# Optimization experiments

Measured on AMD Instinct MI355X. Metric: run time of the kernel, lower is better.

The kernel has to match this reference:

```python
import jax, jax.numpy as jnp
import numpy as np

B, S, H, I = 2, 2048, 2048, 8192

def setup_inputs() -> dict:
    key = jax.random.key(0)
    k1, k2, k3, k4 = jax.random.split(key, 4)
    x = jax.random.normal(k1, (B, S, H), dtype=jnp.float32)
    gate_w = jax.random.normal(k2, (I, H), dtype=jnp.float32) * 0.02
    up_w = jax.random.normal(k3, (I, H), dtype=jnp.float32) * 0.02
    down_w = jax.random.normal(k4, (H, I), dtype=jnp.float32) * 0.02
    return {"x": x, "gate_w": gate_w, "up_w": up_w, "down_w": down_w}

def reference(x, gate_w, up_w, down_w):
    # SwiGLU FFN forward. In the torch module the hybrid compression only
    # affects activations SAVED for backward; forward output is exact F.linear.
    h_gate = jnp.einsum('bsh,ih->bsi', x, gate_w)   # (B,S,I)
    h_up = jnp.einsum('bsh,ih->bsi', x, up_w)       # (B,S,I)
    h_mid = jax.nn.silu(h_gate) * h_up              # (B,S,I)
    y = jnp.einsum('bsi,hi->bsh', h_mid, down_w)    # (B,S,H)
    return y
```

## Files before the change

### kernel.cpp

```cpp
#include <hip/hip_runtime.h>
#include <hip/hip_bf16.h>
#include <stdint.h>

typedef __attribute__((ext_vector_type(4))) float f32x4;
typedef __attribute__((ext_vector_type(8))) short short8;

__device__ __forceinline__ unsigned short f32_to_bf16_rne(float f) {
  union { float f; unsigned int u; } v; v.f = f;
  unsigned int u = v.u;
  unsigned int r = u + 0x7fffu + ((u >> 16) & 1u);
  return (unsigned short)(r >> 16);
}

#define GLOAD16(gp, lp)                                                 \
  __builtin_amdgcn_global_load_lds(                                     \
      (const __attribute__((address_space(1))) void*)(const void*)(gp), \
      (__attribute__((address_space(3))) void*)(void*)(lp), 16, 0, 0)

#define BAR() __builtin_amdgcn_s_barrier()
#define WAIT_LGKM0() asm volatile("s_waitcnt lgkmcnt(0)" ::: "memory")
#define WAIT_VM8() asm volatile("s_waitcnt vmcnt(8)" ::: "memory")
#define WAIT_VM0() asm volatile("s_waitcnt vmcnt(0)" ::: "memory")


__global__ __launch_bounds__(256) void cvt_f32_bf16(const float* __restrict__ in,
                                                    unsigned short* __restrict__ out,
                                                    int n4) {
  int i = blockIdx.x * 256 + threadIdx.x;
  int stride = gridDim.x * 256;
  for (; i < n4; i += stride) {
    float4 v = reinterpret_cast<const float4*>(in)[i];
    ushort4 o;
    o.x = f32_to_bf16_rne(v.x);
    o.y = f32_to_bf16_rne(v.y);
    o.z = f32_to_bf16_rne(v.z);
    o.w = f32_to_bf16_rne(v.w);
    reinterpret_cast<ushort4*>(out)[i] = o;
  }
}

__global__ __launch_bounds__(256) void pack_gateup(const float* __restrict__ g,
                                                   const float* __restrict__ u,
                                                   unsigned short* __restrict__ out) {
  const int n = 16384 * 512;
  int idx = blockIdx.x * 256 + threadIdx.x;
  for (; idx < n; idx += gridDim.x * 256) {
    int R = idx >> 9, h4 = idx & 511;
    int grp = R >> 5, s = R & 31;
    const float* src = (s < 16 ? g : u) + (((size_t)(grp * 16 + (s & 15))) << 11) + (h4 << 2);
    float4 v = *reinterpret_cast<const float4*>(src);
    ushort4 o;
    o.x = f32_to_bf16_rne(v.x);
    o.y = f32_to_bf16_rne(v.y);
    o.z = f32_to_bf16_rne(v.z);
    o.w = f32_to_bf16_rne(v.w);
    *reinterpret_cast<ushort4*>(out + ((size_t)idx << 2)) = o;
  }
}

__global__ __launch_bounds__(256) void reduce_add(const float* __restrict__ a,
                                                  const float* __restrict__ b,
                                                  float* __restrict__ o, int n4) {
  int i = blockIdx.x * 256 + threadIdx.x;
  for (; i < n4; i += gridDim.x * 256) {
    float4 x = reinterpret_cast<const float4*>(a)[i];
    float4 y = reinterpret_cast<const float4*>(b)[i];
    float4 z;
    z.x = x.x + y.x; z.y = x.y + y.y; z.z = x.z + y.z; z.w = x.w + y.w;
    reinterpret_cast<float4*>(o)[i] = z;
  }
}


#define MFMA_Q(MH, NH)                                                        \
  do {                                                                        \
    _Pragma("unroll") for (int kh = 0; kh < 2; ++kh) {                        \
      _Pragma("unroll") for (int mi = 0; mi < 4; ++mi) {                      \
        _Pragma("unroll") for (int ni = 0; ni < 2; ++ni) {                    \
          acc[(MH)*4 + mi][(NH)*2 + ni] =                                     \
              __builtin_amdgcn_mfma_f32_16x16x32_bf16(                        \
                  a[mi][kh], b[(NH)*2 + ni][kh],                              \
                  acc[(MH)*4 + mi][(NH)*2 + ni], 0, 0, 0);                    \
        }                                                                     \
      }                                                                       \
    }                                                                         \
  } while (0)

#define STAGE(MAT, BUF, H, T)                                                 \
  do {                                                                        \
    const unsigned short* p0_ =                                               \
        MAT##base + (size_t)((H)*128 + r0) * ld##MAT + (size_t)(T)*64 + c0;   \
    const unsigned short* p1_ =                                               \
        MAT##base + (size_t)((H)*128 + r1) * ld##MAT + (size_t)(T)*64 + c1;   \
    GLOAD16(p0_, &s##MAT[BUF][H][off0 >> 1]);                                 \
    GLOAD16(p1_, &s##MAT[BUF][H][(off0 >> 1) + 512]);                         \
  } while (0)

#define LDA(dst, BUF, MI, KH)                                                 \
  {                                                                           \
    int lb_ = ((MI)*16 + frow) * 128 + (KH)*64 + kg * 16;                     \
    int ph_ = lb_ ^ ((frow & 7) << 4);                                        \
    dst = *reinterpret_cast<const short8*>(                                   \
        reinterpret_cast<const char*>(&sA[BUF][wr][0]) + ph_);                \
  }

#define LDB(dst, BUF, NI, KH)                                                 \
  {                                                                           \
    int lb_ = ((wc & 1) * 64 + (NI)*16 + frow) * 128 + (KH)*64 + kg * 16;     \
    int ph_ = lb_ ^ ((frow & 7) << 4);                                        \
    dst = *reinterpret_cast<const short8*>(                                   \
        reinterpret_cast<const char*>(&sB[BUF][wc >> 1][0]) + ph_);           \
  }

template <int EPI>
__global__ __launch_bounds__(512, 2) void gemm8p(
    const unsigned short* __restrict__ A, const unsigned short* __restrict__ B,
    void* __restrict__ Cout, int K, int ldA, int ldB, int Nout, size_t zstride,
    int nbm, int nbn) {
  __shared__ unsigned short sA[2][2][128 * 64];
  __shared__ unsigned short sB[2][2][128 * 64];

  const int t = threadIdx.x;
  const int wv = t >> 6, ln = t & 63;
  const int wr = wv >> 2, wc = wv & 3;
  const int frow = ln & 15, kg = ln >> 4;

  const int r = blockIdx.x;
  const int swz = (r & 7) * (gridDim.x >> 3) + (r >> 3);
  const int bm = swz % nbm;
  const int rest = swz / nbm;
  const int bn = rest % nbn;
  const int bz = rest / nbn;

  A += (size_t)bz * K;
  B += (size_t)bz * K;

  const int off0 = wv * 2048 + ln * 16;
  const int off1 = off0 + 1024;
  const int s0 = off0 ^ (((off0 >> 7) & 7) << 4);
  const int s1 = off1 ^ (((off1 >> 7) & 7) << 4);
  const int r0 = s0 >> 7, c0 = (s0 & 127) >> 1;
  const int r1 = s1 >> 7, c1 = (s1 & 127) >> 1;

  const unsigned short* Abase = A + (size_t)(bm * 256) * ldA;
  const unsigned short* Bbase = B + (size_t)(bn * 256) * ldB;

  f32x4 acc[8][4] = {};
  short8 a[4][2], b[4][2];

  const int NT = K >> 6;

  STAGE(A, 0, 0, 0); STAGE(A, 0, 1, 0);
  STAGE(B, 0, 0, 0); STAGE(B, 0, 1, 0);
  STAGE(A, 1, 0, 1); STAGE(A, 1, 1, 1);
  STAGE(B, 1, 0, 1); STAGE(B, 1, 1, 1);
  WAIT_VM8();
  BAR();

  for (int tt = 0; tt < NT; ++tt) {
    const int buf = tt & 1;
#pragma unroll
    for (int mi = 0; mi < 4; ++mi) { LDA(a[mi][0], buf, mi, 0); LDA(a[mi][1], buf, mi, 1); }
#pragma unroll
    for (int ni = 0; ni < 2; ++ni) { LDB(b[ni][0], buf, ni, 0); LDB(b[ni][1], buf, ni, 1); }
    BAR(); WAIT_LGKM0();
    __builtin_amdgcn_s_setprio(1); MFMA_Q(0, 0); __builtin_amdgcn_s_setprio(0);
    BAR();
#pragma unroll
    for (int ni = 2; ni < 4; ++ni) { LDB(b[ni][0], buf, ni, 0); LDB(b[ni][1], buf, ni, 1); }
    BAR(); WAIT_LGKM0();
    __builtin_amdgcn_s_setprio(1); MFMA_Q(0, 1); __builtin_amdgcn_s_setprio(0);
    BAR();
#pragma unroll
    for (int mi = 0; mi < 4; ++mi) { LDA(a[mi][0], buf, mi + 4, 0); LDA(a[mi][1], buf, mi + 4, 1); }
    if (tt + 2 < NT) { STAGE(B, buf, 0, tt + 2); STAGE(B, buf, 1, tt + 2); }
    BAR(); WAIT_LGKM0();
    __builtin_amdgcn_s_setprio(1); MFMA_Q(1, 0); __builtin_amdgcn_s_setprio(0);
    BAR();
    if (tt + 2 < NT) { STAGE(A, buf, 0, tt + 2); STAGE(A, buf, 1, tt + 2); }
    BAR(); WAIT_LGKM0();
    __builtin_amdgcn_s_setprio(1); MFMA_Q(1, 1); __builtin_amdgcn_s_setprio(0);
    if (tt < NT - 1) {
      if (tt + 2 < NT) { WAIT_VM8(); } else { WAIT_VM0(); }
    }
    BAR();
  }

  if (EPI == 0) {
    float* C = reinterpret_cast<float*>(Cout) + (size_t)bz * zstride;
    const int rb = bm * 256 + wr * 128 + kg * 4;
    const int cb = bn * 256 + wc * 64 + frow;
#pragma unroll
    for (int mi = 0; mi < 8; ++mi)
#pragma unroll
      for (int ni = 0; ni < 4; ++ni)
#pragma unroll
        for (int j = 0; j < 4; ++j)
          C[(size_t)(rb + mi * 16 + j) * Nout + (cb + ni * 16)] = acc[mi][ni][j];
  } else {
    unsigned short* Hm = reinterpret_cast<unsigned short*>(Cout);
    const int rb = bm * 256 + wr * 128 + kg * 4;
    const int cb = bn * 128 + wc * 32 + frow;
#pragma unroll
    for (int mi = 0; mi < 8; ++mi)
#pragma unroll
      for (int p = 0; p < 2; ++p)
#pragma unroll
        for (int j = 0; j < 4; ++j) {
          float gg = acc[mi][2 * p][j];
          float uu = acc[mi][2 * p + 1][j];
          float h = gg * uu * __builtin_amdgcn_rcpf(1.0f + __expf(-gg));
          Hm[(size_t)(rb + mi * 16 + j) * Nout + (cb + p * 16)] = f32_to_bf16_rne(h);
        }
  }
}


extern "C" void kernel_launch(void* const* d_in, const int* in_sizes, int n_in,
                              void* d_out, int out_size, void* d_ws, size_t ws_size,
                              hipStream_t stream) {
  const float* x      = (const float*)d_in[0];
  const float* gate_w = (const float*)d_in[1];
  const float* up_w   = (const float*)d_in[2];
  const float* down_w = (const float*)d_in[3];
  float* y = (float*)d_out;

  const int Mtok = 4096, H = 2048, I = 8192;

  unsigned short* x_bf = (unsigned short*)d_ws;
  unsigned short* Bcat = x_bf + (size_t)Mtok * H;
  unsigned short* d_bf = Bcat + (size_t)2 * I * H;
  unsigned short* h_bf = d_bf + (size_t)H * I;
  float* part = (float*)Bcat;

  cvt_f32_bf16<<<2048, 256, 0, stream>>>(down_w, d_bf, (H * I) / 4);
  cvt_f32_bf16<<<2048, 256, 0, stream>>>(x, x_bf, (Mtok * H) / 4);
  pack_gateup<<<2048, 256, 0, stream>>>(gate_w, up_w, Bcat);

  gemm8p<1><<<dim3(1024), 512, 0, stream>>>(
      x_bf, Bcat, h_bf, H, H, H, I, 0, Mtok / 256, (2 * I) / 256);

  gemm8p<0><<<dim3(256), 512, 0, stream>>>(
      h_bf, d_bf, part, I / 2, I, I, H, (size_t)Mtok * H, Mtok / 256, H / 256);

  reduce_add<<<2048, 256, 0, stream>>>(part, part + (size_t)Mtok * H, y,
                                       (Mtok * H) / 4);
}
```

Baseline: 457.6 us.

## Switch GEMM to 32x32x16 MFMA tiles and fuse conversion kernels into one prep

Replaces the 16x16x32 bf16 MFMA inner loop with 32x32x16 MFMAs, changing the LDS fragment loads, the accumulator layout and both epilogues. The gate/up interleave in the packed weight changes from groups of 16 rows to groups of 32 to match the wider N fragment. The three f32-to-bf16 conversion launches are merged into a single prep kernel. The intent is fewer MFMA issues and LDS reads per FLOP, plus less launch overhead. The risk is bank conflicts in the new fragment load pattern and a changed register footprint.

```diff
diff --git a/kernel.cpp b/kernel.cpp
--- a/kernel.cpp
+++ b/kernel.cpp
@@ -3,6 +3,7 @@
 #include <stdint.h>
 
 typedef __attribute__((ext_vector_type(4))) float f32x4;
+typedef __attribute__((ext_vector_type(16))) float f32x16;
 typedef __attribute__((ext_vector_type(8))) short short8;
 
 __device__ __forceinline__ unsigned short f32_to_bf16_rne(float f) {
@@ -22,39 +23,40 @@
 #define WAIT_VM8() asm volatile("s_waitcnt vmcnt(8)" ::: "memory")
 #define WAIT_VM0() asm volatile("s_waitcnt vmcnt(0)" ::: "memory")
 
-
-__global__ __launch_bounds__(256) void cvt_f32_bf16(const float* __restrict__ in,
-                                                    unsigned short* __restrict__ out,
-                                                    int n4) {
+__global__ __launch_bounds__(256) void prep(
+    const float* __restrict__ x, const float* __restrict__ g,
+    const float* __restrict__ u, const float* __restrict__ dw,
+    unsigned short* __restrict__ x_bf, unsigned short* __restrict__ d_bf,
+    unsigned short* __restrict__ Bcat) {
+  const int NX4 = 2097152;
+  const int ND4 = 4194304;
+  const int NP4 = 8388608;
+  const int total = NX4 + ND4 + NP4;
   int i = blockIdx.x * 256 + threadIdx.x;
-  int stride = gridDim.x * 256;
-  for (; i < n4; i += stride) {
-    float4 v = reinterpret_cast<const float4*>(in)[i];
-    ushort4 o;
-    o.x = f32_to_bf16_rne(v.x);
-    o.y = f32_to_bf16_rne(v.y);
-    o.z = f32_to_bf16_rne(v.z);
-    o.w = f32_to_bf16_rne(v.w);
-    reinterpret_cast<ushort4*>(out)[i] = o;
-  }
-}
-
-__global__ __launch_bounds__(256) void pack_gateup(const float* __restrict__ g,
-                                                   const float* __restrict__ u,
-                                                   unsigned short* __restrict__ out) {
-  const int n = 16384 * 512;
-  int idx = blockIdx.x * 256 + threadIdx.x;
-  for (; idx < n; idx += gridDim.x * 256) {
-    int R = idx >> 9, h4 = idx & 511;
-    int grp = R >> 5, s = R & 31;
-    const float* src = (s < 16 ? g : u) + (((size_t)(grp * 16 + (s & 15))) << 11) + (h4 << 2);
+  for (; i < total; i += gridDim.x * 256) {
+    const float* src;
+    unsigned short* dst;
+    if (i < NX4) {
+      src = x + ((size_t)i << 2);
+      dst = x_bf + ((size_t)i << 2);
+    } else if (i < NX4 + ND4) {
+      int j = i - NX4;
+      src = dw + ((size_t)j << 2);
+      dst = d_bf + ((size_t)j << 2);
+    } else {
+      int j = i - NX4 - ND4;
+      int R = j >> 9, h4 = j & 511;
+      int grp = R >> 6, s = R & 63;
+      src = (s < 32 ? g : u) + (((size_t)(grp * 32 + (s & 31))) << 11) + (h4 << 2);
+      dst = Bcat + ((size_t)j << 2);
+    }
     float4 v = *reinterpret_cast<const float4*>(src);
     ushort4 o;
     o.x = f32_to_bf16_rne(v.x);
     o.y = f32_to_bf16_rne(v.y);
     o.z = f32_to_bf16_rne(v.z);
     o.w = f32_to_bf16_rne(v.w);
-    *reinterpret_cast<ushort4*>(out + ((size_t)idx << 2)) = o;
+    *reinterpret_cast<ushort4*>(dst) = o;
   }
 }
 
@@ -72,16 +74,12 @@
 }
 
 
-#define MFMA_Q(MH, NH)                                                        \
+#define MFMA_P(MH, NH)                                                        \
   do {                                                                        \
-    _Pragma("unroll") for (int kh = 0; kh < 2; ++kh) {                        \
-      _Pragma("unroll") for (int mi = 0; mi < 4; ++mi) {                      \
-        _Pragma("unroll") for (int ni = 0; ni < 2; ++ni) {                    \
-          acc[(MH)*4 + mi][(NH)*2 + ni] =                                     \
-              __builtin_amdgcn_mfma_f32_16x16x32_bf16(                        \
-                  a[mi][kh], b[(NH)*2 + ni][kh],                              \
-                  acc[(MH)*4 + mi][(NH)*2 + ni], 0, 0, 0);                    \
-        }                                                                     \
+    _Pragma("unroll") for (int ks = 0; ks < 4; ++ks) {                        \
+      _Pragma("unroll") for (int mp = 0; mp < 2; ++mp) {                      \
+        acc[(MH)*2 + mp][NH] = __builtin_amdgcn_mfma_f32_32x32x16_bf16(       \
+            a[mp][ks], b[NH][ks], acc[(MH)*2 + mp][NH], 0, 0, 0);             \
       }                                                                       \
     }                                                                         \
   } while (0)
@@ -96,18 +94,20 @@
     GLOAD16(p1_, &s##MAT[BUF][H][(off0 >> 1) + 512]);                         \
   } while (0)
 
-#define LDA(dst, BUF, MI, KH)                                                 \
+#define LDA32(dst, BUF, MI, KS)                                               \
   {                                                                           \
-    int lb_ = ((MI)*16 + frow) * 128 + (KH)*64 + kg * 16;                     \
-    int ph_ = lb_ ^ ((frow & 7) << 4);                                        \
+    int row_ = (MI)*32 + (ln & 31);                                           \
+    int lb_ = row_ * 128 + (KS)*32 + ((ln >> 5) << 4);                        \
+    int ph_ = lb_ ^ ((row_ & 7) << 4);                                        \
     dst = *reinterpret_cast<const short8*>(                                   \
         reinterpret_cast<const char*>(&sA[BUF][wr][0]) + ph_);                \
   }
 
-#define LDB(dst, BUF, NI, KH)                                                 \
+#define LDB32(dst, BUF, NI, KS)                                               \
   {                                                                           \
-    int lb_ = ((wc & 1) * 64 + (NI)*16 + frow) * 128 + (KH)*64 + kg * 16;     \
-    int ph_ = lb_ ^ ((frow & 7) << 4);                                        \
+    int row_ = (wc & 1) * 64 + (NI)*32 + (ln & 31);                           \
+    int lb_ = row_ * 128 + (KS)*32 + ((ln >> 5) << 4);                        \
+    int ph_ = lb_ ^ ((row_ & 7) << 4);                                        \
     dst = *reinterpret_cast<const short8*>(                                   \
         reinterpret_cast<const char*>(&sB[BUF][wc >> 1][0]) + ph_);           \
   }
@@ -123,7 +123,6 @@
   const int t = threadIdx.x;
   const int wv = t >> 6, ln = t & 63;
   const int wr = wv >> 2, wc = wv & 3;
-  const int frow = ln & 15, kg = ln >> 4;
 
   const int r = blockIdx.x;
   const int swz = (r & 7) * (gridDim.x >> 3) + (r >> 3);
@@ -145,8 +144,8 @@
   const unsigned short* Abase = A + (size_t)(bm * 256) * ldA;
   const unsigned short* Bbase = B + (size_t)(bn * 256) * ldB;
 
-  f32x4 acc[8][4] = {};
-  short8 a[4][2], b[4][2];
+  f32x16 acc[4][2] = {};
+  short8 a[2][4], b[2][4];
 
   const int NT = K >> 6;
 
@@ -160,26 +159,30 @@
   for (int tt = 0; tt < NT; ++tt) {
     const int buf = tt & 1;
 #pragma unroll
-    for (int mi = 0; mi < 4; ++mi) { LDA(a[mi][0], buf, mi, 0); LDA(a[mi][1], buf, mi, 1); }
-#pragma unroll
-    for (int ni = 0; ni < 2; ++ni) { LDB(b[ni][0], buf, ni, 0); LDB(b[ni][1], buf, ni, 1); }
-    BAR(); WAIT_LGKM0();
-    __builtin_amdgcn_s_setprio(1); MFMA_Q(0, 0); __builtin_amdgcn_s_setprio(0);
-    BAR();
-#pragma unroll
-    for (int ni = 2; ni < 4; ++ni) { LDB(b[ni][0], buf, ni, 0); LDB(b[ni][1], buf, ni, 1); }
-    BAR(); WAIT_LGKM0();
-    __builtin_amdgcn_s_setprio(1); MFMA_Q(0, 1); __builtin_amdgcn_s_setprio(0);
-    BAR();
-#pragma unroll
-    for (int mi = 0; mi < 4; ++mi) { LDA(a[mi][0], buf, mi + 4, 0); LDA(a[mi][1], buf, mi + 4, 1); }
+    for (int mp = 0; mp < 2; ++mp)
+#pragma unroll
+      for (int ks = 0; ks < 4; ++ks) LDA32(a[mp][ks], buf, mp, ks);
+#pragma unroll
+    for (int ks = 0; ks < 4; ++ks) LDB32(b[0][ks], buf, 0, ks);
+    BAR(); WAIT_LGKM0();
+    __builtin_amdgcn_s_setprio(1); MFMA_P(0, 0); __builtin_amdgcn_s_setprio(0);
+    BAR();
+#pragma unroll
+    for (int ks = 0; ks < 4; ++ks) LDB32(b[1][ks], buf, 1, ks);
+    BAR(); WAIT_LGKM0();
+    __builtin_amdgcn_s_setprio(1); MFMA_P(0, 1); __builtin_amdgcn_s_setprio(0);
+    BAR();
+#pragma unroll
+    for (int mp = 0; mp < 2; ++mp)
+#pragma unroll
+      for (int ks = 0; ks < 4; ++ks) LDA32(a[mp][ks], buf, 2 + mp, ks);
     if (tt + 2 < NT) { STAGE(B, buf, 0, tt + 2); STAGE(B, buf, 1, tt + 2); }
     BAR(); WAIT_LGKM0();
-    __builtin_amdgcn_s_setprio(1); MFMA_Q(1, 0); __builtin_amdgcn_s_setprio(0);
+    __builtin_amdgcn_s_setprio(1); MFMA_P(1, 0); __builtin_amdgcn_s_setprio(0);
     BAR();
     if (tt + 2 < NT) { STAGE(A, buf, 0, tt + 2); STAGE(A, buf, 1, tt + 2); }
     BAR(); WAIT_LGKM0();
-    __builtin_amdgcn_s_setprio(1); MFMA_Q(1, 1); __builtin_amdgcn_s_setprio(0);
+    __builtin_amdgcn_s_setprio(1); MFMA_P(1, 1); __builtin_amdgcn_s_setprio(0);
     if (tt < NT - 1) {
       if (tt + 2 < NT) { WAIT_VM8(); } else { WAIT_VM0(); }
     }
@@ -188,30 +191,31 @@
 
   if (EPI == 0) {
     float* C = reinterpret_cast<float*>(Cout) + (size_t)bz * zstride;
-    const int rb = bm * 256 + wr * 128 + kg * 4;
-    const int cb = bn * 256 + wc * 64 + frow;
-#pragma unroll
-    for (int mi = 0; mi < 8; ++mi)
-#pragma unroll
-      for (int ni = 0; ni < 4; ++ni)
-#pragma unroll
-        for (int j = 0; j < 4; ++j)
-          C[(size_t)(rb + mi * 16 + j) * Nout + (cb + ni * 16)] = acc[mi][ni][j];
+    const int rb = bm * 256 + wr * 128 + 4 * (ln >> 5);
+    const int cb = bn * 256 + wc * 64 + (ln & 31);
+#pragma unroll
+    for (int mi = 0; mi < 4; ++mi)
+#pragma unroll
+      for (int nh = 0; nh < 2; ++nh)
+#pragma unroll
+        for (int reg = 0; reg < 16; ++reg) {
+          int row = rb + mi * 32 + (reg & 3) + 8 * (reg >> 2);
+          C[(size_t)row * Nout + cb + nh * 32] = acc[mi][nh][reg];
+        }
   } else {
     unsigned short* Hm = reinterpret_cast<unsigned short*>(Cout);
-    const int rb = bm * 256 + wr * 128 + kg * 4;
-    const int cb = bn * 128 + wc * 32 + frow;
-#pragma unroll
-    for (int mi = 0; mi < 8; ++mi)
-#pragma unroll
-      for (int p = 0; p < 2; ++p)
-#pragma unroll
-        for (int j = 0; j < 4; ++j) {
-          float gg = acc[mi][2 * p][j];
-          float uu = acc[mi][2 * p + 1][j];
-          float h = gg * uu * __builtin_amdgcn_rcpf(1.0f + __expf(-gg));
-          Hm[(size_t)(rb + mi * 16 + j) * Nout + (cb + p * 16)] = f32_to_bf16_rne(h);
-        }
+    const int rb = bm * 256 + wr * 128 + 4 * (ln >> 5);
+    const int cb = bn * 128 + wc * 32 + (ln & 31);
+#pragma unroll
+    for (int mi = 0; mi < 4; ++mi)
+#pragma unroll
+      for (int reg = 0; reg < 16; ++reg) {
+        float gg = acc[mi][0][reg];
+        float uu = acc[mi][1][reg];
+        float h = gg * uu * __builtin_amdgcn_rcpf(1.0f + __expf(-gg));
+        int row = rb + mi * 32 + (reg & 3) + 8 * (reg >> 2);
+        Hm[(size_t)row * Nout + cb] = f32_to_bf16_rne(h);
+      }
   }
 }
 
@@ -233,9 +237,7 @@
   unsigned short* h_bf = d_bf + (size_t)H * I;
   float* part = (float*)Bcat;
 
-  cvt_f32_bf16<<<2048, 256, 0, stream>>>(down_w, d_bf, (H * I) / 4);
-  cvt_f32_bf16<<<2048, 256, 0, stream>>>(x, x_bf, (Mtok * H) / 4);
-  pack_gateup<<<2048, 256, 0, stream>>>(gate_w, up_w, Bcat);
+  prep<<<2048, 256, 0, stream>>>(x, gate_w, up_w, down_w, x_bf, d_bf, Bcat);
 
   gemm8p<1><<<dim3(1024), 512, 0, stream>>>(
       x_bf, Bcat, h_bf, H, H, H, I, 0, Mtok / 256, (2 * I) / 256);
```

New measurement: 501.2 us. 1.1x slower.

## Make gate/up GEMM persistent across tiles and merge prep conversions into one kernel

Applied to the files above, without the earlier changes.

The three fp32-to-bf16 conversion kernels become a single prep kernel, which saves two launches. The first GEMM now runs a persistent grid of 256 workgroups. Each workgroup processes 4 consecutive output tiles in one continuous K loop, so loads for the next tile's first k-slices are issued while the current tile finishes and its epilogue runs. The trade-off is that the epilogue now sits inside the main loop, which adds register pressure and branches, and tile assignment per workgroup changes L2 locality.

```diff
diff --git a/kernel.cpp b/kernel.cpp
--- a/kernel.cpp
+++ b/kernel.cpp
@@ -22,39 +22,40 @@
 #define WAIT_VM8() asm volatile("s_waitcnt vmcnt(8)" ::: "memory")
 #define WAIT_VM0() asm volatile("s_waitcnt vmcnt(0)" ::: "memory")
 
-
-__global__ __launch_bounds__(256) void cvt_f32_bf16(const float* __restrict__ in,
-                                                    unsigned short* __restrict__ out,
-                                                    int n4) {
+__global__ __launch_bounds__(256) void prep(
+    const float* __restrict__ x, const float* __restrict__ g,
+    const float* __restrict__ u, const float* __restrict__ dw,
+    unsigned short* __restrict__ x_bf, unsigned short* __restrict__ d_bf,
+    unsigned short* __restrict__ Bcat) {
+  const int NX4 = 2097152;
+  const int ND4 = 4194304;
+  const int NP4 = 8388608;
+  const int total = NX4 + ND4 + NP4;
   int i = blockIdx.x * 256 + threadIdx.x;
-  int stride = gridDim.x * 256;
-  for (; i < n4; i += stride) {
-    float4 v = reinterpret_cast<const float4*>(in)[i];
-    ushort4 o;
-    o.x = f32_to_bf16_rne(v.x);
-    o.y = f32_to_bf16_rne(v.y);
-    o.z = f32_to_bf16_rne(v.z);
-    o.w = f32_to_bf16_rne(v.w);
-    reinterpret_cast<ushort4*>(out)[i] = o;
-  }
-}
-
-__global__ __launch_bounds__(256) void pack_gateup(const float* __restrict__ g,
-                                                   const float* __restrict__ u,
-                                                   unsigned short* __restrict__ out) {
-  const int n = 16384 * 512;
-  int idx = blockIdx.x * 256 + threadIdx.x;
-  for (; idx < n; idx += gridDim.x * 256) {
-    int R = idx >> 9, h4 = idx & 511;
-    int grp = R >> 5, s = R & 31;
-    const float* src = (s < 16 ? g : u) + (((size_t)(grp * 16 + (s & 15))) << 11) + (h4 << 2);
+  for (; i < total; i += gridDim.x * 256) {
+    const float* src;
+    unsigned short* dst;
+    if (i < NX4) {
+      src = x + ((size_t)i << 2);
+      dst = x_bf + ((size_t)i << 2);
+    } else if (i < NX4 + ND4) {
+      int j = i - NX4;
+      src = dw + ((size_t)j << 2);
+      dst = d_bf + ((size_t)j << 2);
+    } else {
+      int j = i - NX4 - ND4;
+      int R = j >> 9, h4 = j & 511;
+      int grp = R >> 5, s = R & 31;
+      src = (s < 16 ? g : u) + (((size_t)(grp * 16 + (s & 15))) << 11) + (h4 << 2);
+      dst = Bcat + ((size_t)j << 2);
+    }
     float4 v = *reinterpret_cast<const float4*>(src);
     ushort4 o;
     o.x = f32_to_bf16_rne(v.x);
     o.y = f32_to_bf16_rne(v.y);
     o.z = f32_to_bf16_rne(v.z);
     o.w = f32_to_bf16_rne(v.w);
-    *reinterpret_cast<ushort4*>(out + ((size_t)idx << 2)) = o;
+    *reinterpret_cast<ushort4*>(dst) = o;
   }
 }
 
@@ -86,14 +87,24 @@
     }                                                                         \
   } while (0)
 
-#define STAGE(MAT, BUF, H, T)                                                 \
+#define STAGEA(BUF, H, T)                                                     \
   do {                                                                        \
     const unsigned short* p0_ =                                               \
-        MAT##base + (size_t)((H)*128 + r0) * ld##MAT + (size_t)(T)*64 + c0;   \
+        sAb + (size_t)((H)*128 + r0) * ldA + (size_t)(T)*64 + c0;             \
     const unsigned short* p1_ =                                               \
-        MAT##base + (size_t)((H)*128 + r1) * ld##MAT + (size_t)(T)*64 + c1;   \
-    GLOAD16(p0_, &s##MAT[BUF][H][off0 >> 1]);                                 \
-    GLOAD16(p1_, &s##MAT[BUF][H][(off0 >> 1) + 512]);                         \
+        sAb + (size_t)((H)*128 + r1) * ldA + (size_t)(T)*64 + c1;             \
+    GLOAD16(p0_, &sA[BUF][H][off0 >> 1]);                                     \
+    GLOAD16(p1_, &sA[BUF][H][(off0 >> 1) + 512]);                             \
+  } while (0)
+
+#define STAGEB(BUF, H, T)                                                     \
+  do {                                                                        \
+    const unsigned short* p0_ =                                               \
+        sBb + (size_t)((H)*128 + r0) * ldB + (size_t)(T)*64 + c0;             \
+    const unsigned short* p1_ =                                               \
+        sBb + (size_t)((H)*128 + r1) * ldB + (size_t)(T)*64 + c1;             \
+    GLOAD16(p0_, &sB[BUF][H][off0 >> 1]);                                     \
+    GLOAD16(p1_, &sB[BUF][H][(off0 >> 1) + 512]);                             \
   } while (0)
 
 #define LDA(dst, BUF, MI, KH)                                                 \
@@ -116,7 +127,7 @@
 __global__ __launch_bounds__(512, 2) void gemm8p(
     const unsigned short* __restrict__ A, const unsigned short* __restrict__ B,
     void* __restrict__ Cout, int K, int ldA, int ldB, int Nout, size_t zstride,
-    int nbm, int nbn) {
+    int nbm, int nbn, int tpb) {
   __shared__ unsigned short sA[2][2][128 * 64];
   __shared__ unsigned short sB[2][2][128 * 64];
 
@@ -126,14 +137,8 @@
   const int frow = ln & 15, kg = ln >> 4;
 
   const int r = blockIdx.x;
-  const int swz = (r & 7) * (gridDim.x >> 3) + (r >> 3);
-  const int bm = swz % nbm;
-  const int rest = swz / nbm;
-  const int bn = rest % nbn;
-  const int bz = rest / nbn;
-
-  A += (size_t)bz * K;
-  B += (size_t)bz * K;
+  const int lin = (r & 7) * (gridDim.x >> 3) + (r >> 3);
+  const int g0 = lin * tpb;
 
   const int off0 = wv * 2048 + ln * 16;
   const int off1 = off0 + 1024;
@@ -142,23 +147,37 @@
   const int r0 = s0 >> 7, c0 = (s0 & 127) >> 1;
   const int r1 = s1 >> 7, c1 = (s1 & 127) >> 1;
 
-  const unsigned short* Abase = A + (size_t)(bm * 256) * ldA;
-  const unsigned short* Bbase = B + (size_t)(bn * 256) * ldB;
+  int cg = g0;
+  int cbm = cg % nbm, crest = cg / nbm, cbn = crest % nbn, cbz = crest / nbn;
+
+  const unsigned short* sAb = A + (size_t)cbz * K + (size_t)(cbm * 256) * ldA;
+  const unsigned short* sBb = B + (size_t)cbz * K + (size_t)(cbn * 256) * ldB;
+  int sg = cg;
 
   f32x4 acc[8][4] = {};
   short8 a[4][2], b[4][2];
 
   const int NT = K >> 6;
-
-  STAGE(A, 0, 0, 0); STAGE(A, 0, 1, 0);
-  STAGE(B, 0, 0, 0); STAGE(B, 0, 1, 0);
-  STAGE(A, 1, 0, 1); STAGE(A, 1, 1, 1);
-  STAGE(B, 1, 0, 1); STAGE(B, 1, 1, 1);
+  const int total = tpb * NT;
+  int sk = 2, qs = 2;
+  int ck = 0;
+
+  STAGEA(0, 0, 0); STAGEA(0, 1, 0);
+  STAGEB(0, 0, 0); STAGEB(0, 1, 0);
+  STAGEA(1, 0, 1); STAGEA(1, 1, 1);
+  STAGEB(1, 0, 1); STAGEB(1, 1, 1);
   WAIT_VM8();
   BAR();
 
-  for (int tt = 0; tt < NT; ++tt) {
-    const int buf = tt & 1;
+  for (int q = 0; q < total; ++q) {
+    const int buf = q & 1;
+    const bool st = (qs < total);
+    if (st && sk == NT) {
+      sk = 0; ++sg;
+      int sbm = sg % nbm, srest = sg / nbm, sbn = srest % nbn, sbz = srest / nbn;
+      sAb = A + (size_t)sbz * K + (size_t)(sbm * 256) * ldA;
+      sBb = B + (size_t)sbz * K + (size_t)(sbn * 256) * ldB;
+    }
 #pragma unroll
     for (int mi = 0; mi < 4; ++mi) { LDA(a[mi][0], buf, mi, 0); LDA(a[mi][1], buf, mi, 1); }
 #pragma unroll
@@ -173,45 +192,54 @@
     BAR();
 #pragma unroll
     for (int mi = 0; mi < 4; ++mi) { LDA(a[mi][0], buf, mi + 4, 0); LDA(a[mi][1], buf, mi + 4, 1); }
-    if (tt + 2 < NT) { STAGE(B, buf, 0, tt + 2); STAGE(B, buf, 1, tt + 2); }
+    if (st) { STAGEB(buf, 0, sk); STAGEB(buf, 1, sk); }
     BAR(); WAIT_LGKM0();
     __builtin_amdgcn_s_setprio(1); MFMA_Q(1, 0); __builtin_amdgcn_s_setprio(0);
     BAR();
-    if (tt + 2 < NT) { STAGE(A, buf, 0, tt + 2); STAGE(A, buf, 1, tt + 2); }
+    if (st) { STAGEA(buf, 0, sk); STAGEA(buf, 1, sk); ++sk; ++qs; }
     BAR(); WAIT_LGKM0();
     __builtin_amdgcn_s_setprio(1); MFMA_Q(1, 1); __builtin_amdgcn_s_setprio(0);
-    if (tt < NT - 1) {
-      if (tt + 2 < NT) { WAIT_VM8(); } else { WAIT_VM0(); }
+    if (q == total - 2) { WAIT_VM0(); } else if (q < total - 1) { WAIT_VM8(); }
+    BAR();
+
+    if (++ck == NT) {
+      if (EPI == 0) {
+        float* C = reinterpret_cast<float*>(Cout) + (size_t)cbz * zstride;
+        const int rb = cbm * 256 + wr * 128 + kg * 4;
+        const int cb = cbn * 256 + wc * 64 + frow;
+#pragma unroll
+        for (int mi = 0; mi < 8; ++mi)
+#pragma unroll
+          for (int ni = 0; ni < 4; ++ni)
+#pragma unroll
+            for (int j = 0; j < 4; ++j)
+              C[(size_t)(rb + mi * 16 + j) * Nout + (cb + ni * 16)] = acc[mi][ni][j];
+      } else {
+        unsigned short* Hm = reinterpret_cast<unsigned short*>(Cout);
+        const int rb = cbm * 256 + wr * 128 + kg * 4;
+        const int cb = cbn * 128 + wc * 32 + frow;
+#pragma unroll
+        for (int mi = 0; mi < 8; ++mi)
+#pragma unroll
+          for (int p = 0; p < 2; ++p)
+#pragma unroll
+            for (int j = 0; j < 4; ++j) {
+              float gg = acc[mi][2 * p][j];
+              float uu = acc[mi][2 * p + 1][j];
+              float h = gg * uu * __builtin_amdgcn_rcpf(1.0f + __expf(-gg));
+              Hm[(size_t)(rb + mi * 16 + j) * Nout + (cb + p * 16)] = f32_to_bf16_rne(h);
+            }
+      }
+      if (q + 1 < total) {
+        ck = 0; ++cg;
+        cbm = cg % nbm; crest = cg / nbm; cbn = crest % nbn; cbz = crest / nbn;
+#pragma unroll
+        for (int mi = 0; mi < 8; ++mi)
+#pragma unroll
+          for (int ni = 0; ni < 4; ++ni)
+            acc[mi][ni] = (f32x4){0.f, 0.f, 0.f, 0.f};
+      }
     }
-    BAR();
-  }
-
-  if (EPI == 0) {
-    float* C = reinterpret_cast<float*>(Cout) + (size_t)bz * zstride;
-    const int rb = bm * 256 + wr * 128 + kg * 4;
-    const int cb = bn * 256 + wc * 64 + frow;
-#pragma unroll
-    for (int mi = 0; mi < 8; ++mi)
-#pragma unroll
-      for (int ni = 0; ni < 4; ++ni)
-#pragma unroll
-        for (int j = 0; j < 4; ++j)
-          C[(size_t)(rb + mi * 16 + j) * Nout + (cb + ni * 16)] = acc[mi][ni][j];
-  } else {
-    unsigned short* Hm = reinterpret_cast<unsigned short*>(Cout);
-    const int rb = bm * 256 + wr * 128 + kg * 4;
-    const int cb = bn * 128 + wc * 32 + frow;
-#pragma unroll
-    for (int mi = 0; mi < 8; ++mi)
-#pragma unroll
-      for (int p = 0; p < 2; ++p)
-#pragma unroll
-        for (int j = 0; j < 4; ++j) {
-          float gg = acc[mi][2 * p][j];
-          float uu = acc[mi][2 * p + 1][j];
-          float h = gg * uu * __builtin_amdgcn_rcpf(1.0f + __expf(-gg));
-          Hm[(size_t)(rb + mi * 16 + j) * Nout + (cb + p * 16)] = f32_to_bf16_rne(h);
-        }
   }
 }
 
@@ -233,15 +261,13 @@
   unsigned short* h_bf = d_bf + (size_t)H * I;
   float* part = (float*)Bcat;
 
-  cvt_f32_bf16<<<2048, 256, 0, stream>>>(down_w, d_bf, (H * I) / 4);
-  cvt_f32_bf16<<<2048, 256, 0, stream>>>(x, x_bf, (Mtok * H) / 4);
-  pack_gateup<<<2048, 256, 0, stream>>>(gate_w, up_w, Bcat);
-
-  gemm8p<1><<<dim3(1024), 512, 0, stream>>>(
-      x_bf, Bcat, h_bf, H, H, H, I, 0, Mtok / 256, (2 * I) / 256);
+  prep<<<2048, 256, 0, stream>>>(x, gate_w, up_w, down_w, x_bf, d_bf, Bcat);
+
+  gemm8p<1><<<dim3(256), 512, 0, stream>>>(
+      x_bf, Bcat, h_bf, H, H, H, I, 0, Mtok / 256, (2 * I) / 256, 4);
 
   gemm8p<0><<<dim3(256), 512, 0, stream>>>(
-      h_bf, d_bf, part, I / 2, I, I, H, (size_t)Mtok * H, Mtok / 256, H / 256);
+      h_bf, d_bf, part, I / 2, I, I, H, (size_t)Mtok * H, Mtok / 256, H / 256, 1);
 
   reduce_add<<<2048, 256, 0, stream>>>(part, part + (size_t)Mtok * H, y,
                                        (Mtok * H) / 4);
```

Measured after the change: 493.4 us. 1.08x slower.

## Fuse prep conversions, pad leading dimensions, replace split-K reduce with atomics

Applied to the files above, without the earlier changes.

Merges the three f32-to-bf16 conversion kernels into one prep kernel and pads the row strides of the bf16 buffers by 32 elements, which is meant to reduce channel or bank conflicts in the GEMM loads. The split-K down projection now atomically adds both K halves into a zero-initialised output, replacing the partial buffers and the separate reduce_add kernel. This removes launches and a full read and write of the partial sums. In exchange it adds a memset and fp32 atomics, whose summation order is nondeterministic.

```diff
diff --git a/kernel.cpp b/kernel.cpp
--- a/kernel.cpp
+++ b/kernel.cpp
@@ -22,52 +22,42 @@
 #define WAIT_VM8() asm volatile("s_waitcnt vmcnt(8)" ::: "memory")
 #define WAIT_VM0() asm volatile("s_waitcnt vmcnt(0)" ::: "memory")
 
-
-__global__ __launch_bounds__(256) void cvt_f32_bf16(const float* __restrict__ in,
-                                                    unsigned short* __restrict__ out,
-                                                    int n4) {
+__global__ __launch_bounds__(256) void prep(
+    const float* __restrict__ x, const float* __restrict__ g,
+    const float* __restrict__ u, const float* __restrict__ dw,
+    unsigned short* __restrict__ x_bf, unsigned short* __restrict__ d_bf,
+    unsigned short* __restrict__ Bcat, int ldX, int ldD, int ldB) {
+  const int NX4 = 2097152;
+  const int ND4 = 4194304;
+  const int NP4 = 8388608;
+  const int total = NX4 + ND4 + NP4;
   int i = blockIdx.x * 256 + threadIdx.x;
-  int stride = gridDim.x * 256;
-  for (; i < n4; i += stride) {
-    float4 v = reinterpret_cast<const float4*>(in)[i];
-    ushort4 o;
-    o.x = f32_to_bf16_rne(v.x);
-    o.y = f32_to_bf16_rne(v.y);
-    o.z = f32_to_bf16_rne(v.z);
-    o.w = f32_to_bf16_rne(v.w);
-    reinterpret_cast<ushort4*>(out)[i] = o;
-  }
-}
-
-__global__ __launch_bounds__(256) void pack_gateup(const float* __restrict__ g,
-                                                   const float* __restrict__ u,
-                                                   unsigned short* __restrict__ out) {
-  const int n = 16384 * 512;
-  int idx = blockIdx.x * 256 + threadIdx.x;
-  for (; idx < n; idx += gridDim.x * 256) {
-    int R = idx >> 9, h4 = idx & 511;
-    int grp = R >> 5, s = R & 31;
-    const float* src = (s < 16 ? g : u) + (((size_t)(grp * 16 + (s & 15))) << 11) + (h4 << 2);
+  for (; i < total; i += gridDim.x * 256) {
+    const float* src;
+    unsigned short* dst;
+    if (i < NX4) {
+      int m = i >> 9, j = i & 511;
+      src = x + ((size_t)i << 2);
+      dst = x_bf + (size_t)m * ldX + (j << 2);
+    } else if (i < NX4 + ND4) {
+      int j2 = i - NX4;
+      int r_ = j2 >> 11, j = j2 & 2047;
+      src = dw + ((size_t)j2 << 2);
+      dst = d_bf + (size_t)r_ * ldD + (j << 2);
+    } else {
+      int j3 = i - NX4 - ND4;
+      int R = j3 >> 9, h4 = j3 & 511;
+      int grp = R >> 5, s = R & 31;
+      src = (s < 16 ? g : u) + (((size_t)(grp * 16 + (s & 15))) << 11) + (h4 << 2);
+      dst = Bcat + (size_t)R * ldB + (h4 << 2);
+    }
     float4 v = *reinterpret_cast<const float4*>(src);
     ushort4 o;
     o.x = f32_to_bf16_rne(v.x);
     o.y = f32_to_bf16_rne(v.y);
     o.z = f32_to_bf16_rne(v.z);
     o.w = f32_to_bf16_rne(v.w);
-    *reinterpret_cast<ushort4*>(out + ((size_t)idx << 2)) = o;
-  }
-}
-
-__global__ __launch_bounds__(256) void reduce_add(const float* __restrict__ a,
-                                                  const float* __restrict__ b,
-                                                  float* __restrict__ o, int n4) {
-  int i = blockIdx.x * 256 + threadIdx.x;
-  for (; i < n4; i += gridDim.x * 256) {
-    float4 x = reinterpret_cast<const float4*>(a)[i];
-    float4 y = reinterpret_cast<const float4*>(b)[i];
-    float4 z;
-    z.x = x.x + y.x; z.y = x.y + y.y; z.z = x.z + y.z; z.w = x.w + y.w;
-    reinterpret_cast<float4*>(o)[i] = z;
+    *reinterpret_cast<ushort4*>(dst) = o;
   }
 }
 
@@ -115,7 +105,7 @@
 template <int EPI>
 __global__ __launch_bounds__(512, 2) void gemm8p(
     const unsigned short* __restrict__ A, const unsigned short* __restrict__ B,
-    void* __restrict__ Cout, int K, int ldA, int ldB, int Nout, size_t zstride,
+    void* __restrict__ Cout, int K, int ldA, int ldB, int ldC,
     int nbm, int nbn) {
   __shared__ unsigned short sA[2][2][128 * 64];
   __shared__ unsigned short sB[2][2][128 * 64];
@@ -187,7 +177,7 @@
   }
 
   if (EPI == 0) {
-    float* C = reinterpret_cast<float*>(Cout) + (size_t)bz * zstride;
+    float* C = reinterpret_cast<float*>(Cout);
     const int rb = bm * 256 + wr * 128 + kg * 4;
     const int cb = bn * 256 + wc * 64 + frow;
 #pragma unroll
@@ -196,7 +186,8 @@
       for (int ni = 0; ni < 4; ++ni)
 #pragma unroll
         for (int j = 0; j < 4; ++j)
-          C[(size_t)(rb + mi * 16 + j) * Nout + (cb + ni * 16)] = acc[mi][ni][j];
+          atomicAdd(&C[(size_t)(rb + mi * 16 + j) * ldC + (cb + ni * 16)],
+                    acc[mi][ni][j]);
   } else {
     unsigned short* Hm = reinterpret_cast<unsigned short*>(Cout);
     const int rb = bm * 256 + wr * 128 + kg * 4;
@@ -210,7 +201,7 @@
           float gg = acc[mi][2 * p][j];
           float uu = acc[mi][2 * p + 1][j];
           float h = gg * uu * __builtin_amdgcn_rcpf(1.0f + __expf(-gg));
-          Hm[(size_t)(rb + mi * 16 + j) * Nout + (cb + p * 16)] = f32_to_bf16_rne(h);
+          Hm[(size_t)(rb + mi * 16 + j) * ldC + (cb + p * 16)] = f32_to_bf16_rne(h);
         }
   }
 }
@@ -227,22 +218,28 @@
 
   const int Mtok = 4096, H = 2048, I = 8192;
 
+  const int PAD = 32;
+  size_t need = ((size_t)Mtok * (H + PAD) + (size_t)(2 * I) * (H + PAD) +
+                 (size_t)H * (I + PAD) + (size_t)Mtok * (I + PAD)) * 2;
+  const int pad = (ws_size >= need) ? PAD : 0;
+  const int ldX = H + pad;
+  const int ldB = H + pad;
+  const int ldD = I + pad;
+  const int ldH = I + pad;
+
   unsigned short* x_bf = (unsigned short*)d_ws;
-  unsigned short* Bcat = x_bf + (size_t)Mtok * H;
-  unsigned short* d_bf = Bcat + (size_t)2 * I * H;
-  unsigned short* h_bf = d_bf + (size_t)H * I;
-  float* part = (float*)Bcat;
-
-  cvt_f32_bf16<<<2048, 256, 0, stream>>>(down_w, d_bf, (H * I) / 4);
-  cvt_f32_bf16<<<2048, 256, 0, stream>>>(x, x_bf, (Mtok * H) / 4);
-  pack_gateup<<<2048, 256, 0, stream>>>(gate_w, up_w, Bcat);
+  unsigned short* Bcat = x_bf + (size_t)Mtok * ldX;
+  unsigned short* d_bf = Bcat + (size_t)2 * I * ldB;
+  unsigned short* h_bf = d_bf + (size_t)H * ldD;
+
+  hipMemsetAsync(y, 0, (size_t)Mtok * H * sizeof(float), stream);
+
+  prep<<<2048, 256, 0, stream>>>(x, gate_w, up_w, down_w, x_bf, d_bf, Bcat,
+                                 ldX, ldD, ldB);
 
   gemm8p<1><<<dim3(1024), 512, 0, stream>>>(
-      x_bf, Bcat, h_bf, H, H, H, I, 0, Mtok / 256, (2 * I) / 256);
+      x_bf, Bcat, h_bf, H, ldX, ldB, ldH, Mtok / 256, (2 * I) / 256);
 
   gemm8p<0><<<dim3(256), 512, 0, stream>>>(
-      h_bf, d_bf, part, I / 2, I, I, H, (size_t)Mtok * H, Mtok / 256, H / 256);
-
-  reduce_add<<<2048, 256, 0, stream>>>(part, part + (size_t)Mtok * H, y,
-                                       (Mtok * H) / 4);
-}
+      h_bf, d_bf, y, I / 2, ldH, ldD, H, Mtok / 256, H / 256);
+}
```

Result: slower. 529.4 us (+15.7%).
